# Optimization experiments

Hardware: AMD Instinct MI355X
Metric: run time of the kernel (lower is better)

Reference implementation:

```python
import jax, jax.numpy as jnp
import numpy as np

N = 50000

def gcn_conv(x, W, b, src, dst, n):
    # x: [N, Fin], W: [Fin, Fout]; PyG GCNConv: transform then sym-normalized aggregate (self-loops included in src/dst)
    h = x @ W  # [N, Fout]
    deg = jax.ops.segment_sum(jnp.ones_like(dst, dtype=h.dtype), dst, num_segments=n)
    inv_sqrt = jnp.where(deg > 0, jax.lax.rsqrt(deg), 0.0)
    norm = inv_sqrt[src] * inv_sqrt[dst]  # [E+N]
    msg = h[src] * norm[:, None]
    out = jax.ops.segment_sum(msg, dst, num_segments=n)
    return out + b


def setup_inputs() -> dict:
    key = jax.random.key(0)
    ks = jax.random.split(key, 8)
    d_in, d_h, n_exp, E = 64, 64, 16, 800000
    x = jax.random.normal(ks[0], (N, d_in), dtype=jnp.float32)
    edge_index = jax.random.randint(ks[1], (2, E), 0, N, dtype=jnp.int64)
    s = 1.0 / np.sqrt(d_in)
    W1 = jax.random.uniform(ks[2], (d_in, d_h), minval=-s, maxval=s, dtype=jnp.float32)
    b1 = jnp.zeros((d_h,), jnp.float32)
    W2 = jax.random.uniform(ks[3], (d_h, d_h), minval=-s, maxval=s, dtype=jnp.float32)
    b2 = jnp.zeros((d_h,), jnp.float32)
    Wc = jax.random.uniform(ks[4], (d_h, n_exp), minval=-s, maxval=s, dtype=jnp.float32)
    bc = jnp.zeros((n_exp,), jnp.float32)
    return {"x": x, "edge_index": edge_index, "W1": W1, "b1": b1, "W2": W2, "b2": b2, "Wc": Wc, "bc": bc}


def reference(x, edge_index, W1, b1, W2, b2, Wc, bc):
    # add self-loops once (PyG GCNConv default add_self_loops=True)
    loops = jnp.arange(N, dtype=edge_index.dtype)
    src = jnp.concatenate([edge_index[0], loops])
    dst = jnp.concatenate([edge_index[1], loops])
    h = jax.nn.relu(gcn_conv(x, W1, b1, src, dst, N))
    # dropout is identity in eval mode
    h = jax.nn.relu(gcn_conv(h, W2, b2, src, dst, N))
    return h @ Wc + bc
```

## Files before the change

### kernel.cpp

```cpp
#include <hip/hip_runtime.h>
#include <hip/hip_fp16.h>


#define FDIM 64
#define NCLS 16
#define TILE 2048

__global__ __launch_bounds__(256) void k_histB(const int* __restrict__ dst, int E,
                                               int* __restrict__ H, int nblk) {
    __shared__ int h[256];
    int t = threadIdx.x, blk = blockIdx.x;
    h[t] = 0;
    __syncthreads();
    int i0 = blk * TILE;
#pragma unroll
    for (int k = 0; k < TILE / 256; ++k) {
        int i = i0 + k * 256 + t;
        if (i < E) atomicAdd(&h[dst[i] >> 8], 1);
    }
    __syncthreads();
    H[t * nblk + blk] = h[t];
}

__global__ __launch_bounds__(512) void k_scanH(int* __restrict__ H, int nblk, int* __restrict__ btot) {
    __shared__ int s[512];
    int t = threadIdx.x, b = blockIdx.x;
    int v = (t < nblk) ? H[b * nblk + t] : 0;
    s[t] = v;
    __syncthreads();
    for (int off = 1; off < 512; off <<= 1) {
        int add = (t >= off) ? s[t - off] : 0;
        __syncthreads();
        s[t] += add;
        __syncthreads();
    }
    if (t < nblk) H[b * nblk + t] = s[t] - v;
    if (t == 511) btot[b] = s[511];
}

__global__ __launch_bounds__(256) void k_scanB(const int* __restrict__ btot, int nb,
                                               int* __restrict__ bbase, int* __restrict__ row_ptr_n, int E) {
    __shared__ int s[256];
    int t = threadIdx.x;
    int v = (t < nb) ? btot[t] : 0;
    s[t] = v;
    __syncthreads();
    for (int off = 1; off < 256; off <<= 1) {
        int add = (t >= off) ? s[t - off] : 0;
        __syncthreads();
        s[t] += add;
        __syncthreads();
    }
    if (t < nb) bbase[t] = s[t] - v;
    if (t == 0) *row_ptr_n = E;
}

__global__ __launch_bounds__(256) void k_scatA(const int* __restrict__ src, const int* __restrict__ dst,
                                               int E, const int* __restrict__ H, int nblk,
                                               const int* __restrict__ bbase, unsigned* __restrict__ tmp) {
    __shared__ int Hb[256];
    __shared__ int c2[256];
    int t = threadIdx.x, blk = blockIdx.x;
    Hb[t] = bbase[t] + H[t * nblk + blk];
    c2[t] = 0;
    __syncthreads();
    int i0 = blk * TILE;
#pragma unroll
    for (int k = 0; k < TILE / 256; ++k) {
        int i = i0 + k * 256 + t;
        if (i < E) {
            int s = src[i], d = dst[i];
            int b = d >> 8;
            unsigned rec = ((unsigned)(d & 255) << 16) | (unsigned)s;
            int pos = Hb[b] + atomicAdd(&c2[b], 1);
            tmp[pos] = rec;
        }
    }
}

#define COLCAP 8192
__global__ __launch_bounds__(256) void k_binB(const unsigned* __restrict__ tmp,
                                              const int* __restrict__ bbase, const int* __restrict__ btot,
                                              int n, int* __restrict__ row_ptr, float* __restrict__ inv,
                                              unsigned short* __restrict__ col) {
    __shared__ int dcnt[256], s[256], cur[256];
    __shared__ unsigned short colbuf[COLCAP];
    int t = threadIdx.x, b = blockIdx.x;
    int base = bbase[b];
    int cntE = btot[b];
    int node0 = b << 8;
    int nn = min(256, n - node0);
    dcnt[t] = 0;
    __syncthreads();
    for (int i = t; i < cntE; i += 256) atomicAdd(&dcnt[tmp[base + i] >> 16], 1);
    __syncthreads();
    int deg = dcnt[t];
    s[t] = deg;
    __syncthreads();
    for (int off = 1; off < 256; off <<= 1) {
        int add = (t >= off) ? s[t - off] : 0;
        __syncthreads();
        s[t] += add;
        __syncthreads();
    }
    int excl = s[t] - deg;
    if (t < nn) {
        row_ptr[node0 + t] = base + excl;
        inv[node0 + t] = rsqrtf((float)(deg + 1));
    }
    cur[t] = excl;
    __syncthreads();
    for (int i = t; i < cntE; i += 256) {
        unsigned r = tmp[base + i];
        int pos = atomicAdd(&cur[r >> 16], 1);
        unsigned short v = (unsigned short)(r & 0xFFFFu);
        if (pos < COLCAP) colbuf[pos] = v;
        else col[base + pos] = v;
    }
    __syncthreads();
    int lim = min(cntE, COLCAP);
    for (int i = t; i < lim; i += 256) col[base + i] = colbuf[i];
}

__global__ __launch_bounds__(256) void k_gemm64(const float* __restrict__ X, const float* __restrict__ W,
                                                const float* __restrict__ inv, __half* __restrict__ Yh, int n) {
    __shared__ float Ws[FDIM * FDIM];
    int t = threadIdx.x;
    for (int i = t; i < FDIM * FDIM; i += 256) Ws[i] = W[i];
    __syncthreads();
    int idx = blockIdx.x * 256 + t;
    int row = idx >> 2;
    int cg = (idx & 3) * 16;
    if (row >= n) return;
    const float4* xr = (const float4*)(X + row * FDIM);
    float4 xv[16];
#pragma unroll
    for (int i = 0; i < 16; ++i) xv[i] = xr[i];
    float acc[16];
#pragma unroll
    for (int c = 0; c < 16; ++c) acc[c] = 0.f;
#pragma unroll
    for (int i = 0; i < 16; ++i) {
        float xs[4] = {xv[i].x, xv[i].y, xv[i].z, xv[i].w};
#pragma unroll
        for (int j = 0; j < 4; ++j) {
            float xk = xs[j];
            const float* wr = &Ws[(i * 4 + j) * FDIM + cg];
#pragma unroll
            for (int c = 0; c < 16; ++c) acc[c] += xk * wr[c];
        }
    }
    float iv = inv[row];
    unsigned u[8];
#pragma unroll
    for (int i = 0; i < 8; ++i) {
        __half2 hp = __floats2half2_rn(acc[2 * i] * iv, acc[2 * i + 1] * iv);
        u[i] = *(unsigned*)&hp;
    }
    uint4* yo = (uint4*)(Yh + (size_t)row * FDIM + cg);
    yo[0] = make_uint4(u[0], u[1], u[2], u[3]);
    yo[1] = make_uint4(u[4], u[5], u[6], u[7]);
}

template <int FUSED>
__global__ __launch_bounds__(256) void k_agg_t(const __half* __restrict__ Ph, const float* __restrict__ inv,
                                               const int* __restrict__ row_ptr,
                                               const unsigned short* __restrict__ col,
                                               const float* __restrict__ bias,
                                               const float* __restrict__ Wc, const float* __restrict__ bc,
                                               float* __restrict__ out, int n) {
    __shared__ float WcT[FUSED ? (NCLS * FDIM) : 1];
    int t = threadIdx.x;
    if (FUSED) {
        for (int i = t; i < FDIM * NCLS; i += 256) {
            int c = i & 15, f = i >> 4;
            WcT[c * FDIM + f] = Wc[i];
        }
        __syncthreads();
    }
    int lane = t & 63;
    int sub = lane >> 4;
    int fl = lane & 15;
    int wid = t >> 6;
    int node = blockIdx.x * 16 + wid * 4 + sub;
    bool alive = node < n;
    int nodeC = alive ? node : (n - 1);
    float iv = inv[nodeC];
    const uint2* P2 = (const uint2*)Ph;
    uint2 selfq = P2[(size_t)nodeC * 16 + fl];
    __half2 sh0 = *(__half2*)&selfq.x;
    __half2 sh1 = *(__half2*)&selfq.y;
    float2 sf0 = __half22float2(sh0);
    float2 sf1 = __half22float2(sh1);
    float4 acc = make_float4(sf0.x, sf0.y, sf1.x, sf1.y);
    int s = row_ptr[nodeC];
    int e = alive ? row_ptr[nodeC + 1] : s;
    int dmax = e - s;
    dmax = max(dmax, __shfl_xor(dmax, 16, 64));
    dmax = max(dmax, __shfl_xor(dmax, 32, 64));
    for (int j = 0; j < dmax; j += 8) {
        int c[8];
        float wk[8];
        uint2 q[8];
#pragma unroll
        for (int k = 0; k < 8; ++k) {
            int jj = s + j + k;
            bool ok = jj < e;
            c[k] = col[ok ? jj : s];
            wk[k] = ok ? 1.f : 0.f;
        }
#pragma unroll
        for (int k = 0; k < 8; ++k) q[k] = P2[(size_t)c[k] * 16 + fl];
#pragma unroll
        for (int k = 0; k < 8; ++k) {
            __half2 h0 = *(__half2*)&q[k].x;
            __half2 h1 = *(__half2*)&q[k].y;
            float2 f0 = __half22float2(h0);
            float2 f1 = __half22float2(h1);
            acc.x = fmaf(wk[k], f0.x, acc.x);
            acc.y = fmaf(wk[k], f0.y, acc.y);
            acc.z = fmaf(wk[k], f1.x, acc.z);
            acc.w = fmaf(wk[k], f1.y, acc.w);
        }
    }
    float4 bb = ((const float4*)bias)[fl];
    float4 r;
    r.x = fmaxf(fmaf(iv, acc.x, bb.x), 0.f);
    r.y = fmaxf(fmaf(iv, acc.y, bb.y), 0.f);
    r.z = fmaxf(fmaf(iv, acc.z, bb.z), 0.f);
    r.w = fmaxf(fmaf(iv, acc.w, bb.w), 0.f);
    if (!FUSED) {
        if (alive) ((float4*)out)[(size_t)node * 16 + fl] = r;
    } else {
        float part[NCLS];
#pragma unroll
        for (int c = 0; c < NCLS; ++c) {
            float4 wv = ((const float4*)(WcT + c * FDIM))[fl];
            part[c] = fmaf(r.x, wv.x, fmaf(r.y, wv.y, fmaf(r.z, wv.z, r.w * wv.w)));
        }
#pragma unroll
        for (int m = 1; m < 16; m <<= 1) {
#pragma unroll
            for (int c = 0; c < NCLS; ++c) part[c] += __shfl_xor(part[c], m, 64);
        }
        if (alive && fl < 4) {
            float4 bb2 = ((const float4*)bc)[fl];
            float4 o = make_float4(part[fl * 4 + 0] + bb2.x, part[fl * 4 + 1] + bb2.y,
                                   part[fl * 4 + 2] + bb2.z, part[fl * 4 + 3] + bb2.w);
            ((float4*)out)[(size_t)node * 4 + fl] = o;
        }
    }
}

static inline size_t align256(size_t x) { return (x + 255) & ~(size_t)255; }

extern "C" void kernel_launch(void* const* d_in, const int* in_sizes, int n_in,
                              void* d_out, int out_size, void* d_ws, size_t ws_size,
                              hipStream_t stream) {
    const float* x  = (const float*)d_in[0];
    const int*   ei = (const int*)d_in[1];
    const float* W1 = (const float*)d_in[2];
    const float* b1 = (const float*)d_in[3];
    const float* W2 = (const float*)d_in[4];
    const float* b2 = (const float*)d_in[5];
    const float* Wc = (const float*)d_in[6];
    const float* bc = (const float*)d_in[7];
    float* out = (float*)d_out;

    const int n = in_sizes[0] / FDIM;
    const int E = in_sizes[1] / 2;
    const int* src = ei;
    const int* dst = ei + E;

    const int nb = (n + 255) >> 8;
    const int nblk = (E + TILE - 1) / TILE;

    char* w = (char*)d_ws;
    size_t off = 0;
    int* H = (int*)(w + off);        off = align256(off + (size_t)nb * nblk * 4);
    int* btot = (int*)(w + off);     off = align256(off + 256 * 4);
    int* bbase = (int*)(w + off);    off = align256(off + 256 * 4);
    int* row_ptr = (int*)(w + off);  off = align256(off + (size_t)(n + 1) * 4);
    float* inv = (float*)(w + off);  off = align256(off + (size_t)n * 4);
    unsigned* tmp = (unsigned*)(w + off);          off = align256(off + (size_t)E * 4);
    unsigned short* col = (unsigned short*)(w + off); off = align256(off + (size_t)(E + 8) * 2);
    __half* P = (__half*)(w + off);  off = align256(off + (size_t)n * FDIM * 2);
    float* A = (float*)(w + off);    off = align256(off + (size_t)n * FDIM * 4);
    (void)ws_size;

    const int nbG = (n * 4 + 255) / 256;
    const int nbA = (n + 15) / 16;

    k_histB<<<nblk, 256, 0, stream>>>(dst, E, H, nblk);
    k_scanH<<<nb, 512, 0, stream>>>(H, nblk, btot);
    k_scanB<<<1, 256, 0, stream>>>(btot, nb, bbase, row_ptr + n, E);
    k_scatA<<<nblk, 256, 0, stream>>>(src, dst, E, H, nblk, bbase, tmp);
    k_binB<<<nb, 256, 0, stream>>>(tmp, bbase, btot, n, row_ptr, inv, col);

    k_gemm64<<<nbG, 256, 0, stream>>>(x, W1, inv, P, n);
    k_agg_t<0><<<nbA, 256, 0, stream>>>(P, inv, row_ptr, col, b1, nullptr, nullptr, A, n);
    k_gemm64<<<nbG, 256, 0, stream>>>(A, W2, inv, P, n);
    k_agg_t<1><<<nbA, 256, 0, stream>>>(P, inv, row_ptr, col, b2, Wc, bc, out, n);
}
```

Measured before the change: 170.2 us.

## Fuse layer-2 GEMM into layer-1 aggregation and fold block scan into consumers

The layer-1 aggregation kernel now applies bias and ReLU, stages the rows in shared memory and multiplies by W2 in the same kernel, writing fp16 pre-scaled features directly. This removes the fp32 intermediate write and read and one launch. The single-block scan kernel is removed, and each scatter and bin block recomputes the 196-entry prefix over bucket totals itself. The histogram layout is transposed so per-block rows are contiguous. The cost is redundant scan work per block and a 16KB W2 load per aggregation block, which may reduce occupancy.

New measurement: 160.4 us. 5.8% less time.

```diff
diff --git a/kernel.cpp b/kernel.cpp
--- a/kernel.cpp
+++ b/kernel.cpp
@@ -7,7 +7,7 @@
 #define TILE 2048
 
 __global__ __launch_bounds__(256) void k_histB(const int* __restrict__ dst, int E,
-                                               int* __restrict__ H, int nblk) {
+                                               int* __restrict__ H) {
     __shared__ int h[256];
     int t = threadIdx.x, blk = blockIdx.x;
     h[t] = 0;
@@ -19,13 +19,13 @@
         if (i < E) atomicAdd(&h[dst[i] >> 8], 1);
     }
     __syncthreads();
-    H[t * nblk + blk] = h[t];
+    H[blk * 256 + t] = h[t];
 }
 
 __global__ __launch_bounds__(512) void k_scanH(int* __restrict__ H, int nblk, int* __restrict__ btot) {
     __shared__ int s[512];
     int t = threadIdx.x, b = blockIdx.x;
-    int v = (t < nblk) ? H[b * nblk + t] : 0;
+    int v = (t < nblk) ? H[t * 256 + b] : 0;
     s[t] = v;
     __syncthreads();
     for (int off = 1; off < 512; off <<= 1) {
@@ -34,34 +34,28 @@
         s[t] += add;
         __syncthreads();
     }
-    if (t < nblk) H[b * nblk + t] = s[t] - v;
+    if (t < nblk) H[t * 256 + b] = s[t] - v;
     if (t == 511) btot[b] = s[511];
 }
 
-__global__ __launch_bounds__(256) void k_scanB(const int* __restrict__ btot, int nb,
-                                               int* __restrict__ bbase, int* __restrict__ row_ptr_n, int E) {
+__global__ __launch_bounds__(256) void k_scatA(const int* __restrict__ src, const int* __restrict__ dst,
+                                               int E, const int* __restrict__ H,
+                                               const int* __restrict__ btot, int nb,
+                                               unsigned* __restrict__ tmp) {
     __shared__ int s[256];
-    int t = threadIdx.x;
-    int v = (t < nb) ? btot[t] : 0;
-    s[t] = v;
-    __syncthreads();
-    for (int off = 1; off < 256; off <<= 1) {
-        int add = (t >= off) ? s[t - off] : 0;
-        __syncthreads();
-        s[t] += add;
-        __syncthreads();
-    }
-    if (t < nb) bbase[t] = s[t] - v;
-    if (t == 0) *row_ptr_n = E;
-}
-
-__global__ __launch_bounds__(256) void k_scatA(const int* __restrict__ src, const int* __restrict__ dst,
-                                               int E, const int* __restrict__ H, int nblk,
-                                               const int* __restrict__ bbase, unsigned* __restrict__ tmp) {
     __shared__ int Hb[256];
     __shared__ int c2[256];
     int t = threadIdx.x, blk = blockIdx.x;
-    Hb[t] = bbase[t] + H[t * nblk + blk];
+    int v = (t < nb) ? btot[t] : 0;
+    s[t] = v;
+    __syncthreads();
+    for (int off = 1; off < 256; off <<= 1) {
+        int add = (t >= off) ? s[t - off] : 0;
+        __syncthreads();
+        s[t] += add;
+        __syncthreads();
+    }
+    Hb[t] = (s[t] - v) + H[blk * 256 + t];
     c2[t] = 0;
     __syncthreads();
     int i0 = blk * TILE;
@@ -69,9 +63,9 @@
     for (int k = 0; k < TILE / 256; ++k) {
         int i = i0 + k * 256 + t;
         if (i < E) {
-            int s = src[i], d = dst[i];
+            int sv = src[i], d = dst[i];
             int b = d >> 8;
-            unsigned rec = ((unsigned)(d & 255) << 16) | (unsigned)s;
+            unsigned rec = ((unsigned)(d & 255) << 16) | (unsigned)sv;
             int pos = Hb[b] + atomicAdd(&c2[b], 1);
             tmp[pos] = rec;
         }
@@ -80,18 +74,30 @@
 
 #define COLCAP 8192
 __global__ __launch_bounds__(256) void k_binB(const unsigned* __restrict__ tmp,
-                                              const int* __restrict__ bbase, const int* __restrict__ btot,
-                                              int n, int* __restrict__ row_ptr, float* __restrict__ inv,
+                                              const int* __restrict__ btot, int nb,
+                                              int n, int E, int* __restrict__ row_ptr,
+                                              float* __restrict__ inv,
                                               unsigned short* __restrict__ col) {
     __shared__ int dcnt[256], s[256], cur[256];
     __shared__ unsigned short colbuf[COLCAP];
     int t = threadIdx.x, b = blockIdx.x;
-    int base = bbase[b];
+    int v = (t < nb) ? btot[t] : 0;
+    s[t] = v;
+    __syncthreads();
+    for (int off = 1; off < 256; off <<= 1) {
+        int add = (t >= off) ? s[t - off] : 0;
+        __syncthreads();
+        s[t] += add;
+        __syncthreads();
+    }
+    __shared__ int baseS;
+    if (t == b) baseS = s[t] - v;
+    dcnt[t] = 0;
+    __syncthreads();
+    int base = baseS;
     int cntE = btot[b];
     int node0 = b << 8;
     int nn = min(256, n - node0);
-    dcnt[t] = 0;
-    __syncthreads();
     for (int i = t; i < cntE; i += 256) atomicAdd(&dcnt[tmp[base + i] >> 16], 1);
     __syncthreads();
     int deg = dcnt[t];
@@ -108,14 +114,15 @@
         row_ptr[node0 + t] = base + excl;
         inv[node0 + t] = rsqrtf((float)(deg + 1));
     }
+    if (b == 0 && t == 0) row_ptr[n] = E;
     cur[t] = excl;
     __syncthreads();
     for (int i = t; i < cntE; i += 256) {
         unsigned r = tmp[base + i];
         int pos = atomicAdd(&cur[r >> 16], 1);
-        unsigned short v = (unsigned short)(r & 0xFFFFu);
-        if (pos < COLCAP) colbuf[pos] = v;
-        else col[base + pos] = v;
+        unsigned short vv = (unsigned short)(r & 0xFFFFu);
+        if (pos < COLCAP) colbuf[pos] = vv;
+        else col[base + pos] = vv;
     }
     __syncthreads();
     int lim = min(cntE, COLCAP);
@@ -162,36 +169,29 @@
     yo[1] = make_uint4(u[4], u[5], u[6], u[7]);
 }
 
-template <int FUSED>
-__global__ __launch_bounds__(256) void k_agg_t(const __half* __restrict__ Ph, const float* __restrict__ inv,
+__global__ __launch_bounds__(256) void k_aggF1(const __half* __restrict__ Ph, const float* __restrict__ inv,
                                                const int* __restrict__ row_ptr,
                                                const unsigned short* __restrict__ col,
                                                const float* __restrict__ bias,
-                                               const float* __restrict__ Wc, const float* __restrict__ bc,
-                                               float* __restrict__ out, int n) {
-    __shared__ float WcT[FUSED ? (NCLS * FDIM) : 1];
+                                               const float* __restrict__ W2,
+                                               __half* __restrict__ P2, int n) {
+    __shared__ float W2s[FDIM * FDIM];
+    __shared__ float rbuf[16][FDIM + 1];
     int t = threadIdx.x;
-    if (FUSED) {
-        for (int i = t; i < FDIM * NCLS; i += 256) {
-            int c = i & 15, f = i >> 4;
-            WcT[c * FDIM + f] = Wc[i];
-        }
-        __syncthreads();
-    }
+    for (int i = t; i < FDIM * FDIM; i += 256) W2s[i] = W2[i];
     int lane = t & 63;
     int sub = lane >> 4;
     int fl = lane & 15;
     int wid = t >> 6;
-    int node = blockIdx.x * 16 + wid * 4 + sub;
+    int nl = wid * 4 + sub;
+    int node = blockIdx.x * 16 + nl;
     bool alive = node < n;
     int nodeC = alive ? node : (n - 1);
     float iv = inv[nodeC];
-    const uint2* P2 = (const uint2*)Ph;
-    uint2 selfq = P2[(size_t)nodeC * 16 + fl];
-    __half2 sh0 = *(__half2*)&selfq.x;
-    __half2 sh1 = *(__half2*)&selfq.y;
-    float2 sf0 = __half22float2(sh0);
-    float2 sf1 = __half22float2(sh1);
+    const uint2* Pq = (const uint2*)Ph;
+    uint2 selfq = Pq[(size_t)nodeC * 16 + fl];
+    float2 sf0 = __half22float2(*(__half2*)&selfq.x);
+    float2 sf1 = __half22float2(*(__half2*)&selfq.y);
     float4 acc = make_float4(sf0.x, sf0.y, sf1.x, sf1.y);
     int s = row_ptr[nodeC];
     int e = alive ? row_ptr[nodeC + 1] : s;
@@ -210,13 +210,94 @@
             wk[k] = ok ? 1.f : 0.f;
         }
 #pragma unroll
-        for (int k = 0; k < 8; ++k) q[k] = P2[(size_t)c[k] * 16 + fl];
+        for (int k = 0; k < 8; ++k) q[k] = Pq[(size_t)c[k] * 16 + fl];
 #pragma unroll
         for (int k = 0; k < 8; ++k) {
-            __half2 h0 = *(__half2*)&q[k].x;
-            __half2 h1 = *(__half2*)&q[k].y;
-            float2 f0 = __half22float2(h0);
-            float2 f1 = __half22float2(h1);
+            float2 f0 = __half22float2(*(__half2*)&q[k].x);
+            float2 f1 = __half22float2(*(__half2*)&q[k].y);
+            acc.x = fmaf(wk[k], f0.x, acc.x);
+            acc.y = fmaf(wk[k], f0.y, acc.y);
+            acc.z = fmaf(wk[k], f1.x, acc.z);
+            acc.w = fmaf(wk[k], f1.y, acc.w);
+        }
+    }
+    float4 bb = ((const float4*)bias)[fl];
+    rbuf[nl][fl * 4 + 0] = fmaxf(fmaf(iv, acc.x, bb.x), 0.f);
+    rbuf[nl][fl * 4 + 1] = fmaxf(fmaf(iv, acc.y, bb.y), 0.f);
+    rbuf[nl][fl * 4 + 2] = fmaxf(fmaf(iv, acc.z, bb.z), 0.f);
+    rbuf[nl][fl * 4 + 3] = fmaxf(fmaf(iv, acc.w, bb.w), 0.f);
+    __syncthreads();
+    int nl2 = t >> 4;
+    int cg = t & 15;
+    int node2 = blockIdx.x * 16 + nl2;
+    const float* rr = rbuf[nl2];
+    float a0 = 0.f, a1 = 0.f, a2 = 0.f, a3 = 0.f;
+#pragma unroll
+    for (int i = 0; i < FDIM; ++i) {
+        float xk = rr[i];
+        const float* wv = &W2s[i * FDIM + cg * 4];
+        a0 = fmaf(xk, wv[0], a0);
+        a1 = fmaf(xk, wv[1], a1);
+        a2 = fmaf(xk, wv[2], a2);
+        a3 = fmaf(xk, wv[3], a3);
+    }
+    if (node2 < n) {
+        float iv2 = inv[node2];
+        __half2 h0 = __floats2half2_rn(a0 * iv2, a1 * iv2);
+        __half2 h1 = __floats2half2_rn(a2 * iv2, a3 * iv2);
+        uint2 val = make_uint2(*(unsigned*)&h0, *(unsigned*)&h1);
+        ((uint2*)P2)[(size_t)node2 * 16 + cg] = val;
+    }
+}
+
+__global__ __launch_bounds__(256) void k_aggF2(const __half* __restrict__ Ph, const float* __restrict__ inv,
+                                               const int* __restrict__ row_ptr,
+                                               const unsigned short* __restrict__ col,
+                                               const float* __restrict__ bias,
+                                               const float* __restrict__ Wc, const float* __restrict__ bc,
+                                               float* __restrict__ out, int n) {
+    __shared__ float WcT[NCLS * FDIM];
+    int t = threadIdx.x;
+    for (int i = t; i < FDIM * NCLS; i += 256) {
+        int c = i & 15, f = i >> 4;
+        WcT[c * FDIM + f] = Wc[i];
+    }
+    __syncthreads();
+    int lane = t & 63;
+    int sub = lane >> 4;
+    int fl = lane & 15;
+    int wid = t >> 6;
+    int node = blockIdx.x * 16 + wid * 4 + sub;
+    bool alive = node < n;
+    int nodeC = alive ? node : (n - 1);
+    float iv = inv[nodeC];
+    const uint2* Pq = (const uint2*)Ph;
+    uint2 selfq = Pq[(size_t)nodeC * 16 + fl];
+    float2 sf0 = __half22float2(*(__half2*)&selfq.x);
+    float2 sf1 = __half22float2(*(__half2*)&selfq.y);
+    float4 acc = make_float4(sf0.x, sf0.y, sf1.x, sf1.y);
+    int s = row_ptr[nodeC];
+    int e = alive ? row_ptr[nodeC + 1] : s;
+    int dmax = e - s;
+    dmax = max(dmax, __shfl_xor(dmax, 16, 64));
+    dmax = max(dmax, __shfl_xor(dmax, 32, 64));
+    for (int j = 0; j < dmax; j += 8) {
+        int c[8];
+        float wk[8];
+        uint2 q[8];
+#pragma unroll
+        for (int k = 0; k < 8; ++k) {
+            int jj = s + j + k;
+            bool ok = jj < e;
+            c[k] = col[ok ? jj : s];
+            wk[k] = ok ? 1.f : 0.f;
+        }
+#pragma unroll
+        for (int k = 0; k < 8; ++k) q[k] = Pq[(size_t)c[k] * 16 + fl];
+#pragma unroll
+        for (int k = 0; k < 8; ++k) {
+            float2 f0 = __half22float2(*(__half2*)&q[k].x);
+            float2 f1 = __half22float2(*(__half2*)&q[k].y);
             acc.x = fmaf(wk[k], f0.x, acc.x);
             acc.y = fmaf(wk[k], f0.y, acc.y);
             acc.z = fmaf(wk[k], f1.x, acc.z);
@@ -229,26 +310,22 @@
     r.y = fmaxf(fmaf(iv, acc.y, bb.y), 0.f);
     r.z = fmaxf(fmaf(iv, acc.z, bb.z), 0.f);
     r.w = fmaxf(fmaf(iv, acc.w, bb.w), 0.f);
-    if (!FUSED) {
-        if (alive) ((float4*)out)[(size_t)node * 16 + fl] = r;
-    } else {
-        float part[NCLS];
-#pragma unroll
-        for (int c = 0; c < NCLS; ++c) {
-            float4 wv = ((const float4*)(WcT + c * FDIM))[fl];
-            part[c] = fmaf(r.x, wv.x, fmaf(r.y, wv.y, fmaf(r.z, wv.z, r.w * wv.w)));
-        }
-#pragma unroll
-        for (int m = 1; m < 16; m <<= 1) {
-#pragma unroll
-            for (int c = 0; c < NCLS; ++c) part[c] += __shfl_xor(part[c], m, 64);
-        }
-        if (alive && fl < 4) {
-            float4 bb2 = ((const float4*)bc)[fl];
-            float4 o = make_float4(part[fl * 4 + 0] + bb2.x, part[fl * 4 + 1] + bb2.y,
-                                   part[fl * 4 + 2] + bb2.z, part[fl * 4 + 3] + bb2.w);
-            ((float4*)out)[(size_t)node * 4 + fl] = o;
-        }
+    float part[NCLS];
+#pragma unroll
+    for (int c = 0; c < NCLS; ++c) {
+        float4 wv = ((const float4*)(WcT + c * FDIM))[fl];
+        part[c] = fmaf(r.x, wv.x, fmaf(r.y, wv.y, fmaf(r.z, wv.z, r.w * wv.w)));
+    }
+#pragma unroll
+    for (int m = 1; m < 16; m <<= 1) {
+#pragma unroll
+        for (int c = 0; c < NCLS; ++c) part[c] += __shfl_xor(part[c], m, 64);
+    }
+    if (alive && fl < 4) {
+        float4 bb2 = ((const float4*)bc)[fl];
+        float4 o = make_float4(part[fl * 4 + 0] + bb2.x, part[fl * 4 + 1] + bb2.y,
+                               part[fl * 4 + 2] + bb2.z, part[fl * 4 + 3] + bb2.w);
+        ((float4*)out)[(size_t)node * 4 + fl] = o;
     }
 }
 
@@ -277,28 +354,25 @@
 
     char* w = (char*)d_ws;
     size_t off = 0;
-    int* H = (int*)(w + off);        off = align256(off + (size_t)nb * nblk * 4);
+    int* H = (int*)(w + off);        off = align256(off + (size_t)nblk * 256 * 4);
     int* btot = (int*)(w + off);     off = align256(off + 256 * 4);
-    int* bbase = (int*)(w + off);    off = align256(off + 256 * 4);
     int* row_ptr = (int*)(w + off);  off = align256(off + (size_t)(n + 1) * 4);
     float* inv = (float*)(w + off);  off = align256(off + (size_t)n * 4);
-    unsigned* tmp = (unsigned*)(w + off);          off = align256(off + (size_t)E * 4);
+    unsigned* tmp = (unsigned*)(w + off);             off = align256(off + (size_t)E * 4);
     unsigned short* col = (unsigned short*)(w + off); off = align256(off + (size_t)(E + 8) * 2);
-    __half* P = (__half*)(w + off);  off = align256(off + (size_t)n * FDIM * 2);
-    float* A = (float*)(w + off);    off = align256(off + (size_t)n * FDIM * 4);
+    __half* P1 = (__half*)(w + off); off = align256(off + (size_t)n * FDIM * 2);
+    __half* P2 = (__half*)(w + off); off = align256(off + (size_t)n * FDIM * 2);
     (void)ws_size;
 
     const int nbG = (n * 4 + 255) / 256;
     const int nbA = (n + 15) / 16;
 
-    k_histB<<<nblk, 256, 0, stream>>>(dst, E, H, nblk);
+    k_histB<<<nblk, 256, 0, stream>>>(dst, E, H);
     k_scanH<<<nb, 512, 0, stream>>>(H, nblk, btot);
-    k_scanB<<<1, 256, 0, stream>>>(btot, nb, bbase, row_ptr + n, E);
-    k_scatA<<<nblk, 256, 0, stream>>>(src, dst, E, H, nblk, bbase, tmp);
-    k_binB<<<nb, 256, 0, stream>>>(tmp, bbase, btot, n, row_ptr, inv, col);
-
-    k_gemm64<<<nbG, 256, 0, stream>>>(x, W1, inv, P, n);
-    k_agg_t<0><<<nbA, 256, 0, stream>>>(P, inv, row_ptr, col, b1, nullptr, nullptr, A, n);
-    k_gemm64<<<nbG, 256, 0, stream>>>(A, W2, inv, P, n);
-    k_agg_t<1><<<nbA, 256, 0, stream>>>(P, inv, row_ptr, col, b2, Wc, bc, out, n);
-}
+    k_scatA<<<nblk, 256, 0, stream>>>(src, dst, E, H, btot, nb, tmp);
+    k_binB<<<nb, 256, 0, stream>>>(tmp, btot, nb, n, E, row_ptr, inv, col);
+
+    k_gemm64<<<nbG, 256, 0, stream>>>(x, W1, inv, P1, n);
+    k_aggF1<<<nbA, 256, 0, stream>>>(P1, inv, row_ptr, col, b1, W2, P2, n);
+    k_aggF2<<<nbA, 256, 0, stream>>>(P2, inv, row_ptr, col, b2, Wc, bc, out, n);
+}
```
